# Performance work log

Measured on AMD Instinct MI355X. Metric: run time of the kernel, lower is better.

Reference implementation:

```python
import jax, jax.numpy as jnp
import numpy as np

B, S, H, V, T = 32, 128, 256, 32000, 100


def setup_inputs() -> dict:
    key = jax.random.key(0)
    ks = jax.random.split(key, 16)
    s = 1.0 / np.sqrt(H)

    def u(k, shape):
        return jax.random.uniform(k, shape, jnp.float32, -s, s)

    return dict(
        enc_outputs=jax.random.normal(ks[0], (B, S, H), jnp.float32),
        enc_hidden=jax.random.normal(ks[1], (1, B, H), jnp.float32),
        target_tensor=jax.random.randint(ks[2], (B, T), 0, V),
        embedding=u(ks[3], (V, H)),
        Qw=u(ks[4], (H, H)), Qb=u(ks[5], (H,)),
        Kw=u(ks[6], (H, H)), Kb=u(ks[7], (H,)),
        Vw=u(ks[8], (1, H)), Vb=u(ks[9], (1,)),
        W_ih=u(ks[10], (3 * H, 2 * H)), W_hh=u(ks[11], (3 * H, H)),
        b_ih=u(ks[12], (3 * H,)), b_hh=u(ks[13], (3 * H,)),
        out_w=u(ks[14], (V, H)), out_b=u(ks[15], (V,)),
    )


def reference(enc_outputs, enc_hidden, target_tensor, embedding,
              Qw, Qb, Kw, Kb, Vw, Vb, W_ih, W_hh, b_ih, b_hh, out_w, out_b):
    # Teacher-forcing decode: dec_input starts at token 0, then target[:, i].
    Bv, Sv, Hd = enc_outputs.shape
    Tv = target_tensor.shape[1]
    # K(keys) is step-invariant: precompute once (same math as in-loop Linear).
    enc_k = enc_outputs @ Kw.T + Kb  # (B,S,H)
    tokens = jnp.concatenate(
        [jnp.zeros((Bv, 1), target_tensor.dtype), target_tensor[:, :-1]], axis=1)
    tokens_t = tokens.T  # (T,B)

    def step(h, tok):
        emb = embedding[tok]                                  # (B,H), dropout=eval noop
        q = h @ Qw.T + Qb                                     # query from hidden
        e = jnp.tanh(q[:, None, :] + enc_k)                   # (B,S,H) additive attn
        scores = jnp.einsum('bsh,h->bs', e, Vw[0]) + Vb[0]    # (B,S)
        w = jax.nn.softmax(scores, axis=-1)
        ctx = jnp.einsum('bs,bsh->bh', w, enc_outputs)        # bmm(weights, keys)
        x = jnp.concatenate([emb, ctx], axis=-1)              # (B,2H)
        gi = x @ W_ih.T + b_ih
        gh = h @ W_hh.T + b_hh
        r = jax.nn.sigmoid(gi[:, :Hd] + gh[:, :Hd])
        z = jax.nn.sigmoid(gi[:, Hd:2 * Hd] + gh[:, Hd:2 * Hd])
        n = jnp.tanh(gi[:, 2 * Hd:] + r * gh[:, 2 * Hd:])
        h_new = (1.0 - z) * n + z * h                         # torch GRU cell
        logits = h_new @ out_w.T + out_b                      # (B,V)
        return h_new, (logits, w)

    h_final, (logits, atts) = jax.lax.scan(step, enc_hidden[0], tokens_t)
    dec_outputs = jax.nn.log_softmax(jnp.transpose(logits, (1, 0, 2)), axis=-1)  # (B,T,V)
    atts = jnp.transpose(atts, (1, 0, 2))                     # (B,T,S)
    return dec_outputs, h_final[None], atts
```

## Files before the change

kernel.cpp:

```cpp
#include <hip/hip_runtime.h>
#include <hip/hip_bf16.h>

#define Bn 32
#define Sn 128
#define Hn 256
#define Vn 32000
#define Tn 100
#define GIn 768
#define AGENT __HIP_MEMORY_SCOPE_AGENT

typedef __attribute__((ext_vector_type(8))) short bf16x8;
typedef __attribute__((ext_vector_type(4))) float f32x4;

__device__ __forceinline__ float frcp(float x){ return __builtin_amdgcn_rcpf(x); }
__device__ __forceinline__ float ftanh(float x){ return 1.0f - 2.0f*frcp(__expf(2.0f*x)+1.0f); }
__device__ __forceinline__ float fsigm(float x){ return frcp(1.0f + __expf(-x)); }
__device__ __forceinline__ float b2f(unsigned short u){
  unsigned int v = ((unsigned int)u) << 16; return __builtin_bit_cast(float, v);
}
__device__ __forceinline__ unsigned short f2bu(float f){
  unsigned int u = __builtin_bit_cast(unsigned int, f);
  u += 0x7FFFu + ((u >> 16) & 1u);
  return (unsigned short)(u >> 16);
}
__device__ __forceinline__ void st_ag_u(unsigned int* p, unsigned int v){
  __hip_atomic_store(p, v, __ATOMIC_RELAXED, AGENT);
}
__device__ __forceinline__ unsigned int ld_ag_u(unsigned int* p){
  return __hip_atomic_load(p, __ATOMIC_RELAXED, AGENT);
}

__global__ __launch_bounds__(256) void k_tr(const float* __restrict__ in,
    float* __restrict__ out, int R, int C)
{
  __shared__ float tile[32][33];
  const int bx = blockIdx.x*32, by = blockIdx.y*32;
  const int tx = threadIdx.x & 31, ty = threadIdx.x >> 5;
  #pragma unroll
  for(int r = ty; r < 32; r += 8)
    if(by + r < R && bx + tx < C) tile[r][tx] = in[(size_t)(by + r)*C + bx + tx];
  __syncthreads();
  #pragma unroll
  for(int r = ty; r < 32; r += 8)
    if(bx + r < C && by + tx < R) out[(size_t)(bx + r)*R + by + tx] = tile[tx][r];
}

__global__ __launch_bounds__(256) void k_packW1R(const float* __restrict__ Qw,
    const float* __restrict__ Whh, unsigned short* __restrict__ W1R)
{
  const int tid = blockIdx.x*256 + threadIdx.x;
  const int lane = tid & 63;
  const int fragid = tid >> 6;
  const int tt = fragid % 5;
  const int kk = (fragid/5) % 8;
  const int w  = (fragid/40) % 8;
  const int hb = fragid/320;
  const int lr = lane & 15, lg = lane >> 4;
  const float* src;
  if(tt < 2){
    const int f = w*32 + tt*16 + lr;
    src = Qw + (size_t)f*Hn;
  } else {
    const int lf = w*48 + (tt-2)*16 + lr;
    const int g = lf >> 7, jj = lf & 127;
    src = Whh + (size_t)(g*256 + hb*128 + jj)*Hn;
  }
  const int col = kk*32 + lg*8;
  float4 v0 = *(const float4*)(src + col), v1 = *(const float4*)(src + col + 4);
  unsigned short* d = W1R + ((size_t)fragid*64 + lane)*8;
  d[0]=f2bu(v0.x); d[1]=f2bu(v0.y); d[2]=f2bu(v0.z); d[3]=f2bu(v0.w);
  d[4]=f2bu(v1.x); d[5]=f2bu(v1.y); d[6]=f2bu(v1.z); d[7]=f2bu(v1.w);
}

__global__ __launch_bounds__(256) void k_cvt(const float* __restrict__ src,
    __hip_bfloat16* __restrict__ dst, int n)
{
  int i = (blockIdx.x*256 + threadIdx.x)*4;
  if(i < n){
    float4 v = *(const float4*)(src + i);
    dst[i+0] = __float2bfloat16(v.x);
    dst[i+1] = __float2bfloat16(v.y);
    dst[i+2] = __float2bfloat16(v.z);
    dst[i+3] = __float2bfloat16(v.w);
  }
}

__global__ __launch_bounds__(256) void k_enc2(const float* __restrict__ enc_outputs,
    const float* __restrict__ KwT, const float* __restrict__ Kb,
    unsigned short* __restrict__ enc_kb16)
{
  const int r0 = blockIdx.x*16, j = threadIdx.x;
  __shared__ __align__(16) float encl[Hn][20];
  #pragma unroll
  for(int r = 0; r < 16; r++) encl[j][r] = enc_outputs[(size_t)(r0 + r)*Hn + j];
  __syncthreads();
  float acc[16];
  #pragma unroll
  for(int r = 0; r < 16; r++) acc[r] = Kb[j];
  for(int d = 0; d < Hn; d++){
    const float wv = KwT[(size_t)d*Hn + j];
    const float4 e0 = *(const float4*)&encl[d][0];
    const float4 e1 = *(const float4*)&encl[d][4];
    const float4 e2 = *(const float4*)&encl[d][8];
    const float4 e3 = *(const float4*)&encl[d][12];
    acc[0]+=e0.x*wv; acc[1]+=e0.y*wv; acc[2]+=e0.z*wv; acc[3]+=e0.w*wv;
    acc[4]+=e1.x*wv; acc[5]+=e1.y*wv; acc[6]+=e1.z*wv; acc[7]+=e1.w*wv;
    acc[8]+=e2.x*wv; acc[9]+=e2.y*wv; acc[10]+=e2.z*wv; acc[11]+=e2.w*wv;
    acc[12]+=e3.x*wv; acc[13]+=e3.y*wv; acc[14]+=e3.z*wv; acc[15]+=e3.w*wv;
  }
  #pragma unroll
  for(int r = 0; r < 16; r++) enc_kb16[(size_t)(r0 + r)*Hn + j] = f2bu(acc[r]);
}

__global__ __launch_bounds__(256) void k_packEk(const unsigned short* __restrict__ enc_kb16,
    unsigned short* __restrict__ ekP)
{
  const int tid = blockIdx.x*256 + threadIdx.x;
  const int b = tid >> 12;
  const int o = tid & 4095;
  const int g = o >> 6, l = o & 63;
  const int w = g >> 3, i = g & 7;
  const int s = w*16 + (l >> 2);
  const int e0 = i*32 + (l & 3)*8;
  const int4 v = *(const int4*)(enc_kb16 + ((size_t)(b*Sn + s))*Hn + e0);
  *(int4*)(ekP + (size_t)b*32768 + (size_t)o*8) = v;
}

__global__ __launch_bounds__(768) void k_encW2b(const float* __restrict__ enc_outputs,
    const float* __restrict__ W_ihT, unsigned short* __restrict__ encW2P)
{
  const int r0 = blockIdx.x*16, tid = threadIdx.x;
  __shared__ __align__(16) float encl[Hn][20];
  if(tid < Hn){
    #pragma unroll
    for(int r = 0; r < 16; r++) encl[tid][r] = enc_outputs[(size_t)(r0 + r)*Hn + tid];
  }
  __syncthreads();
  float acc[16];
  #pragma unroll
  for(int r = 0; r < 16; r++) acc[r] = 0.f;
  for(int d = 0; d < Hn; d++){
    const float wv = W_ihT[(size_t)(Hn + d)*GIn + tid];
    const float4 e0 = *(const float4*)&encl[d][0];
    const float4 e1 = *(const float4*)&encl[d][4];
    const float4 e2 = *(const float4*)&encl[d][8];
    const float4 e3 = *(const float4*)&encl[d][12];
    acc[0]+=e0.x*wv; acc[1]+=e0.y*wv; acc[2]+=e0.z*wv; acc[3]+=e0.w*wv;
    acc[4]+=e1.x*wv; acc[5]+=e1.y*wv; acc[6]+=e1.z*wv; acc[7]+=e1.w*wv;
    acc[8]+=e2.x*wv; acc[9]+=e2.y*wv; acc[10]+=e2.z*wv; acc[11]+=e2.w*wv;
    acc[12]+=e3.x*wv; acc[13]+=e3.y*wv; acc[14]+=e3.z*wv; acc[15]+=e3.w*wv;
  }
  const int g = tid >> 8, jj = tid & 255;
  const int hb = jj >> 7, c = g*128 + (jj & 127);
  #pragma unroll
  for(int r = 0; r < 16; r++){
    const int bs = r0 + r;
    const int bb = bs >> 7, ss = bs & 127;
    encW2P[(((size_t)bb*2 + hb)*384 + c)*128 + ss] = f2bu(acc[r]);
  }
}

__global__ __launch_bounds__(768) void k_giemb2(const int* __restrict__ target,
    const float* __restrict__ embedding, const float* __restrict__ W_ihT,
    const float* __restrict__ b_ih, float* __restrict__ gi_emb)
{
  const int r0 = blockIdx.x*16, tid = threadIdx.x;
  __shared__ __align__(16) float embl[Hn][20];
  if(tid < Hn){
    #pragma unroll
    for(int r = 0; r < 16; r++){
      const int row = r0 + r;
      const int t = row >> 5, b = row & 31;
      const int tok = (t == 0) ? 0 : target[b*Tn + (t-1)];
      embl[tid][r] = embedding[(size_t)tok*Hn + tid];
    }
  }
  __syncthreads();
  float acc[16];
  #pragma unroll
  for(int r = 0; r < 16; r++) acc[r] = b_ih[tid];
  for(int d = 0; d < Hn; d++){
    const float wv = W_ihT[(size_t)d*GIn + tid];
    const float4 e0 = *(const float4*)&embl[d][0];
    const float4 e1 = *(const float4*)&embl[d][4];
    const float4 e2 = *(const float4*)&embl[d][8];
    const float4 e3 = *(const float4*)&embl[d][12];
    acc[0]+=e0.x*wv; acc[1]+=e0.y*wv; acc[2]+=e0.z*wv; acc[3]+=e0.w*wv;
    acc[4]+=e1.x*wv; acc[5]+=e1.y*wv; acc[6]+=e1.z*wv; acc[7]+=e1.w*wv;
    acc[8]+=e2.x*wv; acc[9]+=e2.y*wv; acc[10]+=e2.z*wv; acc[11]+=e2.w*wv;
    acc[12]+=e3.x*wv; acc[13]+=e3.y*wv; acc[14]+=e3.z*wv; acc[15]+=e3.w*wv;
  }
  #pragma unroll
  for(int r = 0; r < 16; r++) gi_emb[(size_t)(r0 + r)*GIn + tid] = acc[r];
}

__global__ __launch_bounds__(512, 2) void k_loop5(
    const float* __restrict__ enc_hidden,
    const unsigned short* __restrict__ ekP,
    const unsigned short* __restrict__ encW2P,
    const unsigned short* __restrict__ W1R,
    const float* __restrict__ Qb, const float* __restrict__ b_hh,
    const float* __restrict__ Vw, const float* __restrict__ Vb,
    const float* __restrict__ gi_emb,
    __hip_bfloat16* __restrict__ h_all,
    float* __restrict__ atts_out,
    float* __restrict__ hfin_out,
    unsigned int* hbuf,
    unsigned int* hflag)
{
  const int p = blockIdx.x >> 1, hb = blockIdx.x & 1, b = p;
  const int tid = threadIdx.x;
  const int lane = tid & 63, wv = tid >> 6;
  const int lr = lane & 15, lg = lane >> 4;

  __shared__ __align__(16) unsigned short ek_l[32768];
  __shared__ __align__(16) unsigned short ew_l[32768];
  __shared__ __align__(16) float h_sh[128];
  __shared__ __align__(16) short h_b16[Hn];
  __shared__ __align__(16) float qgh_sh[1024];
  __shared__ __align__(16) float vw_sh[Hn];
  __shared__ __align__(16) float sc_sh[Sn];
  __shared__ __align__(16) float w_sh[Sn];
  __shared__ __align__(16) float gic_l[384];

  {
    const unsigned short* src = ekP + (size_t)b*32768;
    #pragma unroll
    for(int c = 0; c < 8; c++){
      const int idx = (c*512 + tid)*8;
      *(int4*)(ek_l + idx) = *(const int4*)(src + idx);
    }
  }
  {
    const unsigned short* src = encW2P + ((size_t)(b*2 + hb)*384)*128;
    #pragma unroll
    for(int i = 0; i < 8; i++){
      const int id = i*512 + tid;
      const int c = id >> 4, sg = id & 15;
      *(int4*)(ew_l + c*128 + ((sg ^ (c & 15)) << 3)) =
          *(const int4*)(src + (size_t)c*128 + sg*8);
    }
  }
  bf16x8 er0, er1, er2, er3;
  {
    const unsigned short* esrc = encW2P +
        ((size_t)((b*2 + hb)*384 + 256 + (tid >> 2)))*128 + (tid & 3)*32;
    er0 = *(const bf16x8*)(esrc);
    er1 = *(const bf16x8*)(esrc + 8);
    er2 = *(const bf16x8*)(esrc + 16);
    er3 = *(const bf16x8*)(esrc + 24);
  }
  bf16x8 w1f[40];
  {
    const unsigned short* wsrc = W1R + (((size_t)(hb*8 + wv)*40)*64 + lane)*8;
    #pragma unroll
    for(int f = 0; f < 40; f++) w1f[f] = *(const bf16x8*)(wsrc + (size_t)f*512);
  }
  float bias_r[5]; int idx_r[5];
  #pragma unroll
  for(int tt = 0; tt < 2; tt++){
    const int f = wv*32 + tt*16 + lr;
    bias_r[tt] = Qb[f]; idx_r[tt] = f;
  }
  #pragma unroll
  for(int tt = 2; tt < 5; tt++){
    const int lf = wv*48 + (tt-2)*16 + lr;
    const int g = lf >> 7, jj = lf & 127;
    bias_r[tt] = b_hh[g*256 + hb*128 + jj];
    idx_r[tt]  = 256 + g*256 + hb*128 + jj;
  }
  if(tid < Hn){
    float hv = enc_hidden[b*Hn + tid];
    h_b16[tid] = (short)f2bu(hv);
    vw_sh[tid] = Vw[tid];
  }
  if(tid < 128) h_sh[tid] = enc_hidden[b*Hn + hb*128 + tid];
  __syncthreads();
  const float vb0 = Vb[0];
  const int s2 = tid >> 2, g2 = tid & 3;

  for(int t = 0; t < Tn; t++){
    const int par = t & 1;
    {
      f32x4 acc[5];
      #pragma unroll
      for(int tt = 0; tt < 5; tt++) acc[tt] = (f32x4){0.f,0.f,0.f,0.f};
      #pragma unroll
      for(int kk = 0; kk < 8; kk++){
        bf16x8 a = *(const bf16x8*)(h_b16 + kk*32 + lg*8);
        #pragma unroll
        for(int tt = 0; tt < 5; tt++)
          acc[tt] = __builtin_amdgcn_mfma_f32_16x16x32_bf16(a, w1f[kk*5 + tt], acc[tt], 0, 0, 0);
      }
      if(lane < 16){
        #pragma unroll
        for(int tt = 0; tt < 5; tt++)
          qgh_sh[idx_r[tt]] = acc[tt][0] + bias_r[tt];
      }
    }
    __syncthreads();

    {
      float pacc = 0.f;
      #pragma unroll
      for(int i = 0; i < 8; i++){
        bf16x8 e8 = *(const bf16x8*)(ek_l + ((wv*8 + i) << 9) + lane*8);
        const int kb = i*32 + g2*8;
        #pragma unroll
        for(int j = 0; j < 8; j++){
          float ev = b2f((unsigned short)e8[j]);
          pacc = fmaf(vw_sh[kb + j], ftanh(qgh_sh[kb + j] + ev), pacc);
        }
      }
      pacc += __shfl_xor(pacc, 1); pacc += __shfl_xor(pacc, 2);
      if(g2 == 0) sc_sh[s2] = pacc + vb0;
    }
    __syncthreads();

    if(tid < 64){
      float v0 = sc_sh[tid], v1 = sc_sh[tid + 64];
      float m = fmaxf(v0, v1);
      #pragma unroll
      for(int off = 1; off < 64; off <<= 1) m = fmaxf(m, __shfl_xor(m, off));
      float e0 = __expf(v0 - m), e1 = __expf(v1 - m);
      float sm = e0 + e1;
      #pragma unroll
      for(int off = 1; off < 64; off <<= 1) sm += __shfl_xor(sm, off);
      float inv = frcp(sm);
      float w0 = e0*inv, w1 = e1*inv;
      w_sh[tid] = w0; w_sh[tid + 64] = w1;
      if(hb == 0){
        float* ao = atts_out + ((size_t)b*Tn + t)*Sn;
        ao[tid] = w0; ao[tid + 64] = w1;
      }
    }
    __syncthreads();

    float ge0 = 0.f, ge1 = 0.f, ge2 = 0.f;
    if(tid < 128){
      const float* ge = gi_emb + ((size_t)t*Bn + b)*GIn + hb*128 + tid;
      ge0 = ge[0]; ge1 = ge[256]; ge2 = ge[512];
    }

    {
      const int c3 = tid >> 1, s3 = tid & 1;
      float a3 = 0.f;
      #pragma unroll
      for(int i = 0; i < 8; i++){
        bf16x8 e = *(const bf16x8*)(ew_l + c3*128 + ((((s3 << 3) + i) ^ (c3 & 15)) << 3));
        const float4 wa = *(const float4*)&w_sh[s3*64 + i*8];
        const float4 wb = *(const float4*)&w_sh[s3*64 + i*8 + 4];
        a3 = fmaf(wa.x, b2f((unsigned short)e[0]), a3);
        a3 = fmaf(wa.y, b2f((unsigned short)e[1]), a3);
        a3 = fmaf(wa.z, b2f((unsigned short)e[2]), a3);
        a3 = fmaf(wa.w, b2f((unsigned short)e[3]), a3);
        a3 = fmaf(wb.x, b2f((unsigned short)e[4]), a3);
        a3 = fmaf(wb.y, b2f((unsigned short)e[5]), a3);
        a3 = fmaf(wb.z, b2f((unsigned short)e[6]), a3);
        a3 = fmaf(wb.w, b2f((unsigned short)e[7]), a3);
      }
      a3 += __shfl_xor(a3, 1);
      if(!(tid & 1)) gic_l[c3] = a3;
      const float* wq = &w_sh[(tid & 3)*32];
      float r2 = 0.f;
      #pragma unroll
      for(int j = 0; j < 8; j++) r2 = fmaf(wq[j],      b2f((unsigned short)er0[j]), r2);
      #pragma unroll
      for(int j = 0; j < 8; j++) r2 = fmaf(wq[8 + j],  b2f((unsigned short)er1[j]), r2);
      #pragma unroll
      for(int j = 0; j < 8; j++) r2 = fmaf(wq[16 + j], b2f((unsigned short)er2[j]), r2);
      #pragma unroll
      for(int j = 0; j < 8; j++) r2 = fmaf(wq[24 + j], b2f((unsigned short)er3[j]), r2);
      r2 += __shfl_xor(r2, 1); r2 += __shfl_xor(r2, 2);
      if(!(tid & 3)) gic_l[256 + (tid >> 2)] = r2;
    }
    __syncthreads();

    if(tid < 128){
      float gr = ge0 + gic_l[tid];
      float gz = ge1 + gic_l[128 + tid];
      float gn = ge2 + gic_l[256 + tid];
      const int jg = hb*128 + tid;
      float r = fsigm(gr + qgh_sh[256 + jg]);
      float z = fsigm(gz + qgh_sh[512 + jg]);
      float n = ftanh(gn + r*qgh_sh[768 + jg]);
      float hn2 = (1.0f - z)*n + z*h_sh[tid];
      h_sh[tid] = hn2;
      const unsigned short hb16 = f2bu(hn2);
      h_b16[jg] = (short)hb16;
      h_all[((size_t)t*Bn + b)*Hn + jg] = __float2bfloat16(hn2);
      if(t == Tn-1) hfin_out[b*Hn + jg] = hn2;
      if(t < Tn-1){
        float hnx = __shfl_down(hn2, 1);
        if(!(tid & 1)){
          unsigned int u = (unsigned int)hb16 | ((unsigned int)f2bu(hnx) << 16);
          st_ag_u(&hbuf[((size_t)(par*32 + p)*2 + hb)*64 + (tid >> 1)], u);
        }
      }
    }
    __syncthreads();

    if(t < Tn-1){
      if(tid == 0){
        __hip_atomic_store(&hflag[p*2 + hb], (unsigned)(t + 1), __ATOMIC_RELEASE, AGENT);
        long cnt = 0;
        while(__hip_atomic_load(&hflag[p*2 + (hb^1)], __ATOMIC_ACQUIRE, AGENT) < (unsigned)(t + 1)
              && ++cnt < 10000000L){}
      }
      __syncthreads();
      if(tid < 64){
        unsigned int u = ld_ag_u(&hbuf[((size_t)(par*32 + p)*2 + (hb^1))*64 + tid]);
        ((unsigned int*)h_b16)[(hb^1)*64 + tid] = u;
      }
      __syncthreads();
    }
  }
}

__global__ __launch_bounds__(512, 2) void k_logits2(
    const short* __restrict__ h_all, const short* __restrict__ w_bf,
    const float* __restrict__ out_b,
    float* __restrict__ pmax, float* __restrict__ psum,
    const float* __restrict__ lse, float* __restrict__ dec_out,
    int pass)
{
  const int tid = threadIdx.x;
  const int wave = tid >> 6, lane = tid & 63;
  const int lr = lane & 15, lg = lane >> 4;
  const int wm = wave >> 2, wn = wave & 3;
  const int n0 = blockIdx.x*256 + wn*64;
  const int m0 = blockIdx.y*256 + wm*128;
  f32x4 acc[8][4];
  #pragma unroll
  for(int mt = 0; mt < 8; mt++)
    #pragma unroll
    for(int nt = 0; nt < 4; nt++) acc[mt][nt] = (f32x4){0.f,0.f,0.f,0.f};
  #pragma unroll
  for(int kk = 0; kk < 8; kk++){
    bf16x8 am[8], bn[4];
    #pragma unroll
    for(int mt = 0; mt < 8; mt++){
      int row = m0 + mt*16 + lr; row = row < 3200 ? row : 3199;
      am[mt] = *(const bf16x8*)(h_all + (size_t)row*Hn + kk*32 + lg*8);
    }
    #pragma unroll
    for(int nt = 0; nt < 4; nt++)
      bn[nt] = *(const bf16x8*)(w_bf + (size_t)(n0 + nt*16 + lr)*Hn + kk*32 + lg*8);
    #pragma unroll
    for(int mt = 0; mt < 8; mt++)
      #pragma unroll
      for(int nt = 0; nt < 4; nt++)
        acc[mt][nt] = __builtin_amdgcn_mfma_f32_16x16x32_bf16(am[mt], bn[nt], acc[mt][nt], 0, 0, 0);
  }
  float bias[4];
  #pragma unroll
  for(int nt = 0; nt < 4; nt++) bias[nt] = out_b[n0 + nt*16 + lr];

  if(pass == 0){
    __shared__ float pm_l[256][4];
    __shared__ float ps_l[256][4];
    #pragma unroll
    for(int mt = 0; mt < 8; mt++){
      #pragma unroll
      for(int i = 0; i < 4; i++){
        float v0 = acc[mt][0][i] + bias[0], v1 = acc[mt][1][i] + bias[1];
        float v2 = acc[mt][2][i] + bias[2], v3 = acc[mt][3][i] + bias[3];
        float m = fmaxf(fmaxf(v0, v1), fmaxf(v2, v3));
        m = fmaxf(m, __shfl_xor(m, 1)); m = fmaxf(m, __shfl_xor(m, 2));
        m = fmaxf(m, __shfl_xor(m, 4)); m = fmaxf(m, __shfl_xor(m, 8));
        float s = __expf(v0 - m) + __expf(v1 - m) + __expf(v2 - m) + __expf(v3 - m);
        s += __shfl_xor(s, 1); s += __shfl_xor(s, 2);
        s += __shfl_xor(s, 4); s += __shfl_xor(s, 8);
        if(lr == 0){
          const int rl = wm*128 + mt*16 + lg*4 + i;
          pm_l[rl][wn] = m; ps_l[rl][wn] = s;
        }
      }
    }
    __syncthreads();
    if(tid < 256){
      const int rg = blockIdx.y*256 + tid;
      if(rg < 3200){
        float m = fmaxf(fmaxf(pm_l[tid][0], pm_l[tid][1]), fmaxf(pm_l[tid][2], pm_l[tid][3]));
        float s = ps_l[tid][0]*__expf(pm_l[tid][0] - m) + ps_l[tid][1]*__expf(pm_l[tid][1] - m)
                + ps_l[tid][2]*__expf(pm_l[tid][2] - m) + ps_l[tid][3]*__expf(pm_l[tid][3] - m);
        pmax[(size_t)blockIdx.x*3200 + rg] = m;
        psum[(size_t)blockIdx.x*3200 + rg] = s;
      }
    }
  } else {
    #pragma unroll
    for(int mt = 0; mt < 8; mt++){
      #pragma unroll
      for(int i = 0; i < 4; i++){
        const int rg = blockIdx.y*256 + wm*128 + mt*16 + lg*4 + i;
        if(rg < 3200){
          const float l = lse[rg];
          const int bb = rg & 31, tt2 = rg >> 5;
          float* dst = dec_out + (size_t)bb*((size_t)Tn*Vn) + (size_t)tt2*Vn + n0;
          dst[ 0 + lr] = acc[mt][0][i] + bias[0] - l;
          dst[16 + lr] = acc[mt][1][i] + bias[1] - l;
          dst[32 + lr] = acc[mt][2][i] + bias[2] - l;
          dst[48 + lr] = acc[mt][3][i] + bias[3] - l;
        }
      }
    }
  }
}

__global__ __launch_bounds__(256) void k_lse(const float* __restrict__ pmax,
    const float* __restrict__ psum, float* __restrict__ lse)
{
  const int row = blockIdx.x*256 + threadIdx.x;
  if(row >= Tn*Bn) return;
  float m = -3.0e38f;
  for(int c = 0; c < 125; c++) m = fmaxf(m, pmax[(size_t)c*3200 + row]);
  float s = 0.f;
  for(int c = 0; c < 125; c++)
    s += psum[(size_t)c*3200 + row] * __expf(pmax[(size_t)c*3200 + row] - m);
  lse[row] = m + __logf(s);
}

extern "C" void kernel_launch(void* const* d_in, const int* in_sizes, int n_in,
                              void* d_out, int out_size, void* d_ws, size_t ws_size,
                              hipStream_t stream)
{
  const float* enc_outputs = (const float*)d_in[0];
  const float* enc_hidden  = (const float*)d_in[1];
  const int*   target      = (const int*)d_in[2];
  const float* embedding   = (const float*)d_in[3];
  const float* Qw   = (const float*)d_in[4];
  const float* Qb   = (const float*)d_in[5];
  const float* Kw   = (const float*)d_in[6];
  const float* Kb   = (const float*)d_in[7];
  const float* Vw   = (const float*)d_in[8];
  const float* Vb   = (const float*)d_in[9];
  const float* W_ih = (const float*)d_in[10];
  const float* W_hh = (const float*)d_in[11];
  const float* b_ih = (const float*)d_in[12];
  const float* b_hh = (const float*)d_in[13];
  const float* out_w = (const float*)d_in[14];
  const float* out_b = (const float*)d_in[15];

  float* dec  = (float*)d_out;
  float* hfin = dec + (size_t)Bn*Tn*Vn;
  float* atts = hfin + Bn*Hn;

  unsigned short* enc_kb16 = (unsigned short*)(dec);
  unsigned short* ekP      = (unsigned short*)(dec + 524288);
  unsigned short* encW2P   = (unsigned short*)(dec + 1048576);
  float* gi_emb = dec + 2621440;
  float* W_ihT  = dec + 5079040;
  float* KwT    = dec + 5472256;
  float* pmax   = dec + 5537792;
  float* psum   = dec + 5937792;
  unsigned short* W1R = (unsigned short*)(dec + 6337792);
  unsigned int* hbuf  = (unsigned int*)(dec + 6501632);
  unsigned int* hflag = (unsigned int*)(dec + 6509824);

  float* wsf = (float*)d_ws;
  float* lse = wsf;
  __hip_bfloat16* h_all = (__hip_bfloat16*)(wsf + 3200);
  __hip_bfloat16* w_bf  = h_all + (size_t)Tn*Bn*Hn;

  k_tr     <<<dim3(8, 8),   dim3(256), 0, stream>>>(Kw, KwT, 256, 256);
  k_tr     <<<dim3(16, 24), dim3(256), 0, stream>>>(W_ih, W_ihT, 768, 512);
  k_packW1R<<<dim3(160),    dim3(256), 0, stream>>>(Qw, W_hh, W1R);
  k_cvt    <<<dim3((Vn*Hn)/1024), dim3(256), 0, stream>>>(out_w, w_bf, Vn*Hn);
  k_enc2   <<<dim3(256), dim3(256), 0, stream>>>(enc_outputs, KwT, Kb, enc_kb16);
  k_packEk <<<dim3(512), dim3(256), 0, stream>>>(enc_kb16, ekP);
  k_encW2b <<<dim3(256), dim3(768), 0, stream>>>(enc_outputs, W_ihT, encW2P);
  k_giemb2 <<<dim3(200), dim3(768), 0, stream>>>(target, embedding, W_ihT, b_ih, gi_emb);

  hipMemsetAsync((void*)hflag, 0, 64*sizeof(unsigned int), stream);

  k_loop5 <<<dim3(64), dim3(512), 0, stream>>>(enc_hidden, ekP, encW2P, W1R,
            Qb, b_hh, Vw, Vb, gi_emb, h_all, atts, hfin, hbuf, hflag);

  k_logits2<<<dim3(125, 13), dim3(512), 0, stream>>>(
            (const short*)h_all, (const short*)w_bf, out_b,
            pmax, psum, (const float*)nullptr, (float*)nullptr, 0);
  k_lse    <<<dim3(13), dim3(256), 0, stream>>>(pmax, psum, lse);
  k_logits2<<<dim3(125, 13), dim3(512), 0, stream>>>(
            (const short*)h_all, (const short*)w_bf, out_b,
            (float*)nullptr, (float*)nullptr, lse, dec, 1);
}
```

Before: 1.373 ms.

## Split attention scores across block pair and use MFMA for context projection

Each pair of blocks now splits the 128 sequence positions so each block computes attention scores for 64 positions, exchanging partial scores through a global buffer with a second flag. The hidden-state exchange is moved so the local half of the Q/W_hh matvec runs before waiting on the partner, overlapping the sync with compute. The context-times-W_ih projection is recast as MFMA over a fragment-packed layout, which removes the packEk kernel. Block-to-pair mapping is also permuted so paired blocks sit further apart. The change adds a second cross-block handshake per step in exchange for halving the tanh work.

After: 2.068 ms. +50.6%, slower.

```diff
diff --git a/kernel.cpp b/kernel.cpp
--- a/kernel.cpp
+++ b/kernel.cpp
@@ -112,22 +112,8 @@
   for(int r = 0; r < 16; r++) enc_kb16[(size_t)(r0 + r)*Hn + j] = f2bu(acc[r]);
 }
 
-__global__ __launch_bounds__(256) void k_packEk(const unsigned short* __restrict__ enc_kb16,
-    unsigned short* __restrict__ ekP)
-{
-  const int tid = blockIdx.x*256 + threadIdx.x;
-  const int b = tid >> 12;
-  const int o = tid & 4095;
-  const int g = o >> 6, l = o & 63;
-  const int w = g >> 3, i = g & 7;
-  const int s = w*16 + (l >> 2);
-  const int e0 = i*32 + (l & 3)*8;
-  const int4 v = *(const int4*)(enc_kb16 + ((size_t)(b*Sn + s))*Hn + e0);
-  *(int4*)(ekP + (size_t)b*32768 + (size_t)o*8) = v;
-}
-
-__global__ __launch_bounds__(768) void k_encW2b(const float* __restrict__ enc_outputs,
-    const float* __restrict__ W_ihT, unsigned short* __restrict__ encW2P)
+__global__ __launch_bounds__(768) void k_encW2F(const float* __restrict__ enc_outputs,
+    const float* __restrict__ W_ihT, unsigned short* __restrict__ encW2F)
 {
   const int r0 = blockIdx.x*16, tid = threadIdx.x;
   __shared__ __align__(16) float encl[Hn][20];
@@ -151,12 +137,17 @@
     acc[12]+=e3.x*wv; acc[13]+=e3.y*wv; acc[14]+=e3.z*wv; acc[15]+=e3.w*wv;
   }
   const int g = tid >> 8, jj = tid & 255;
-  const int hb = jj >> 7, c = g*128 + (jj & 127);
+  const int hb = jj >> 7, jl = jj & 127;
+  const int c = g*128 + jl;
+  const int wvv = c/48, rem = c - wvv*48, tt = rem >> 4, lr = rem & 15;
   #pragma unroll
   for(int r = 0; r < 16; r++){
     const int bs = r0 + r;
-    const int bb = bs >> 7, ss = bs & 127;
-    encW2P[(((size_t)bb*2 + hb)*384 + c)*128 + ss] = f2bu(acc[r]);
+    const int bb = bs >> 7, s = bs & 127;
+    const int kk = s >> 5, lg = (s >> 3) & 3, e = s & 7;
+    const int lane = lg*16 + lr;
+    encW2F[(size_t)(bb*2 + hb)*49152 + (size_t)((wvv*12 + tt*4 + kk)*64 + lane)*8 + e]
+        = f2bu(acc[r]);
   }
 }
 
@@ -194,10 +185,10 @@
   for(int r = 0; r < 16; r++) gi_emb[(size_t)(r0 + r)*GIn + tid] = acc[r];
 }
 
-__global__ __launch_bounds__(512, 2) void k_loop5(
+__global__ __launch_bounds__(512, 2) void k_loop6(
     const float* __restrict__ enc_hidden,
-    const unsigned short* __restrict__ ekP,
-    const unsigned short* __restrict__ encW2P,
+    const unsigned short* __restrict__ enc_kb16,
+    const unsigned short* __restrict__ encW2F,
     const unsigned short* __restrict__ W1R,
     const float* __restrict__ Qb, const float* __restrict__ b_hh,
     const float* __restrict__ Vw, const float* __restrict__ Vb,
@@ -206,49 +197,44 @@
     float* __restrict__ atts_out,
     float* __restrict__ hfin_out,
     unsigned int* hbuf,
-    unsigned int* hflag)
-{
-  const int p = blockIdx.x >> 1, hb = blockIdx.x & 1, b = p;
+    unsigned int* sbuf,
+    unsigned int* hflag,
+    unsigned int* sflag)
+{
+  const int bid = blockIdx.x;
+  const int hb = (bid >> 3) & 1;
+  const int p  = (bid & 7) | ((bid >> 4) << 3);
+  const int b = p;
   const int tid = threadIdx.x;
   const int lane = tid & 63, wv = tid >> 6;
   const int lr = lane & 15, lg = lane >> 4;
 
-  __shared__ __align__(16) unsigned short ek_l[32768];
-  __shared__ __align__(16) unsigned short ew_l[32768];
+  __shared__ __align__(16) unsigned short ek_l[64*256];
+  __shared__ __align__(16) unsigned short ew_l[49152];
   __shared__ __align__(16) float h_sh[128];
-  __shared__ __align__(16) short h_b16[Hn];
+  __shared__ __align__(16) unsigned short hown_l[128];
   __shared__ __align__(16) float qgh_sh[1024];
   __shared__ __align__(16) float vw_sh[Hn];
   __shared__ __align__(16) float sc_sh[Sn];
   __shared__ __align__(16) float w_sh[Sn];
+  __shared__ __align__(16) unsigned short wb_l[Sn];
   __shared__ __align__(16) float gic_l[384];
 
   {
-    const unsigned short* src = ekP + (size_t)b*32768;
-    #pragma unroll
-    for(int c = 0; c < 8; c++){
+    const unsigned short* src = enc_kb16 + ((size_t)b*Sn + hb*64)*Hn;
+    #pragma unroll
+    for(int c = 0; c < 4; c++){
       const int idx = (c*512 + tid)*8;
       *(int4*)(ek_l + idx) = *(const int4*)(src + idx);
     }
   }
   {
-    const unsigned short* src = encW2P + ((size_t)(b*2 + hb)*384)*128;
-    #pragma unroll
-    for(int i = 0; i < 8; i++){
-      const int id = i*512 + tid;
-      const int c = id >> 4, sg = id & 15;
-      *(int4*)(ew_l + c*128 + ((sg ^ (c & 15)) << 3)) =
-          *(const int4*)(src + (size_t)c*128 + sg*8);
-    }
-  }
-  bf16x8 er0, er1, er2, er3;
-  {
-    const unsigned short* esrc = encW2P +
-        ((size_t)((b*2 + hb)*384 + 256 + (tid >> 2)))*128 + (tid & 3)*32;
-    er0 = *(const bf16x8*)(esrc);
-    er1 = *(const bf16x8*)(esrc + 8);
-    er2 = *(const bf16x8*)(esrc + 16);
-    er3 = *(const bf16x8*)(esrc + 24);
+    const unsigned short* src = encW2F + (size_t)(b*2 + hb)*49152;
+    #pragma unroll
+    for(int c = 0; c < 12; c++){
+      const int idx = (c*512 + tid)*8;
+      *(int4*)(ew_l + idx) = *(const int4*)(src + idx);
+    }
   }
   bf16x8 w1f[40];
   {
@@ -269,56 +255,107 @@
     bias_r[tt] = b_hh[g*256 + hb*128 + jj];
     idx_r[tt]  = 256 + g*256 + hb*128 + jj;
   }
-  if(tid < Hn){
-    float hv = enc_hidden[b*Hn + tid];
-    h_b16[tid] = (short)f2bu(hv);
-    vw_sh[tid] = Vw[tid];
-  }
-  if(tid < 128) h_sh[tid] = enc_hidden[b*Hn + hb*128 + tid];
+  if(tid < Hn) vw_sh[tid] = Vw[tid];
+  if(tid < 128){
+    float hv = enc_hidden[b*Hn + hb*128 + tid];
+    h_sh[tid] = hv; hown_l[tid] = f2bu(hv);
+  }
+  if(tid < 64){
+    float h0 = enc_hidden[b*Hn + hb*128 + tid*2];
+    float h1 = enc_hidden[b*Hn + hb*128 + tid*2 + 1];
+    unsigned int u = (unsigned int)f2bu(h0) | ((unsigned int)f2bu(h1) << 16);
+    st_ag_u(&hbuf[((size_t)(0*32 + p)*2 + hb)*64 + tid], u);
+  }
   __syncthreads();
+  if(tid == 0)
+    __hip_atomic_store(&hflag[p*2 + hb], 1u, __ATOMIC_RELEASE, AGENT);
+
   const float vb0 = Vb[0];
-  const int s2 = tid >> 2, g2 = tid & 3;
+  const int sl = wv*8 + (lane >> 3), g2 = lane & 7;
+  const unsigned short* ekrow = ek_l + sl*256 + g2*32;
 
   for(int t = 0; t < Tn; t++){
     const int par = t & 1;
+    f32x4 acc[5];
+    #pragma unroll
+    for(int tt = 0; tt < 5; tt++) acc[tt] = (f32x4){0.f,0.f,0.f,0.f};
+    #pragma unroll
+    for(int kkl = 0; kkl < 4; kkl++){
+      bf16x8 a = *(const bf16x8*)(hown_l + kkl*32 + lg*8);
+      const int kf = (hb*4 + kkl)*5;
+      #pragma unroll
+      for(int tt = 0; tt < 5; tt++)
+        acc[tt] = __builtin_amdgcn_mfma_f32_16x16x32_bf16(a, w1f[kf + tt], acc[tt], 0, 0, 0);
+    }
     {
-      f32x4 acc[5];
-      #pragma unroll
-      for(int tt = 0; tt < 5; tt++) acc[tt] = (f32x4){0.f,0.f,0.f,0.f};
-      #pragma unroll
-      for(int kk = 0; kk < 8; kk++){
-        bf16x8 a = *(const bf16x8*)(h_b16 + kk*32 + lg*8);
+      long cnt = 0;
+      while(__hip_atomic_load(&hflag[p*2 + (hb^1)], __ATOMIC_ACQUIRE, AGENT) < (unsigned)(t + 1)
+            && ++cnt < 10000000L){}
+    }
+    {
+      unsigned int* hsrc = hbuf + ((size_t)(par*32 + p)*2 + (hb^1))*64;
+      #pragma unroll
+      for(int kkl = 0; kkl < 4; kkl++){
+        unsigned int u0 = ld_ag_u(hsrc + kkl*16 + lg*4);
+        unsigned int u1 = ld_ag_u(hsrc + kkl*16 + lg*4 + 1);
+        unsigned int u2 = ld_ag_u(hsrc + kkl*16 + lg*4 + 2);
+        unsigned int u3 = ld_ag_u(hsrc + kkl*16 + lg*4 + 3);
+        bf16x8 a;
+        a[0]=(short)(u0&0xFFFF); a[1]=(short)(u0>>16);
+        a[2]=(short)(u1&0xFFFF); a[3]=(short)(u1>>16);
+        a[4]=(short)(u2&0xFFFF); a[5]=(short)(u2>>16);
+        a[6]=(short)(u3&0xFFFF); a[7]=(short)(u3>>16);
+        const int kf = ((1-hb)*4 + kkl)*5;
         #pragma unroll
         for(int tt = 0; tt < 5; tt++)
-          acc[tt] = __builtin_amdgcn_mfma_f32_16x16x32_bf16(a, w1f[kk*5 + tt], acc[tt], 0, 0, 0);
-      }
-      if(lane < 16){
-        #pragma unroll
-        for(int tt = 0; tt < 5; tt++)
-          qgh_sh[idx_r[tt]] = acc[tt][0] + bias_r[tt];
-      }
+          acc[tt] = __builtin_amdgcn_mfma_f32_16x16x32_bf16(a, w1f[kf + tt], acc[tt], 0, 0, 0);
+      }
+    }
+    if(lane < 16){
+      #pragma unroll
+      for(int tt = 0; tt < 5; tt++)
+        qgh_sh[idx_r[tt]] = acc[tt][0] + bias_r[tt];
     }
     __syncthreads();
 
     {
       float pacc = 0.f;
       #pragma unroll
-      for(int i = 0; i < 8; i++){
-        bf16x8 e8 = *(const bf16x8*)(ek_l + ((wv*8 + i) << 9) + lane*8);
-        const int kb = i*32 + g2*8;
+      for(int c = 0; c < 4; c++){
+        bf16x8 e8 = *(const bf16x8*)(ekrow + c*8);
+        const int kb = g2*32 + c*8;
         #pragma unroll
         for(int j = 0; j < 8; j++){
           float ev = b2f((unsigned short)e8[j]);
           pacc = fmaf(vw_sh[kb + j], ftanh(qgh_sh[kb + j] + ev), pacc);
         }
       }
-      pacc += __shfl_xor(pacc, 1); pacc += __shfl_xor(pacc, 2);
-      if(g2 == 0) sc_sh[s2] = pacc + vb0;
+      pacc += __shfl_xor(pacc, 1); pacc += __shfl_xor(pacc, 2); pacc += __shfl_xor(pacc, 4);
+      if(g2 == 0){
+        const float sv = pacc + vb0;
+        sc_sh[hb*64 + sl] = sv;
+        st_ag_u(&sbuf[((size_t)(par*32 + p)*2 + hb)*64 + sl],
+                __builtin_bit_cast(unsigned int, sv));
+      }
+    }
+    float ge0 = 0.f, ge1 = 0.f, ge2 = 0.f;
+    if(tid < 128){
+      const float* ge = gi_emb + ((size_t)t*Bn + b)*GIn + hb*128 + tid;
+      ge0 = ge[0]; ge1 = ge[256]; ge2 = ge[512];
     }
     __syncthreads();
+    if(tid == 0)
+      __hip_atomic_store(&sflag[p*2 + hb], (unsigned)(t + 1), __ATOMIC_RELEASE, AGENT);
 
     if(tid < 64){
-      float v0 = sc_sh[tid], v1 = sc_sh[tid + 64];
+      long cnt = 0;
+      while(__hip_atomic_load(&sflag[p*2 + (hb^1)], __ATOMIC_ACQUIRE, AGENT) < (unsigned)(t + 1)
+            && ++cnt < 10000000L){}
+      unsigned int uo = ld_ag_u(&sbuf[((size_t)(par*32 + p)*2 + (hb^1))*64 + tid]);
+      float vo = __builtin_bit_cast(float, uo);
+      float vmine = sc_sh[hb*64 + tid];
+      float v0 = hb ? vo : vmine;
+      float v1 = hb ? vmine : vo;
       float m = fmaxf(v0, v1);
       #pragma unroll
       for(int off = 1; off < 64; off <<= 1) m = fmaxf(m, __shfl_xor(m, off));
@@ -329,6 +366,7 @@
       float inv = frcp(sm);
       float w0 = e0*inv, w1 = e1*inv;
       w_sh[tid] = w0; w_sh[tid + 64] = w1;
+      wb_l[tid] = f2bu(w0); wb_l[tid + 64] = f2bu(w1);
       if(hb == 0){
         float* ao = atts_out + ((size_t)b*Tn + t)*Sn;
         ao[tid] = w0; ao[tid + 64] = w1;
@@ -336,43 +374,21 @@
     }
     __syncthreads();
 
-    float ge0 = 0.f, ge1 = 0.f, ge2 = 0.f;
-    if(tid < 128){
-      const float* ge = gi_emb + ((size_t)t*Bn + b)*GIn + hb*128 + tid;
-      ge0 = ge[0]; ge1 = ge[256]; ge2 = ge[512];
-    }
-
     {
-      const int c3 = tid >> 1, s3 = tid & 1;
-      float a3 = 0.f;
-      #pragma unroll
-      for(int i = 0; i < 8; i++){
-        bf16x8 e = *(const bf16x8*)(ew_l + c3*128 + ((((s3 << 3) + i) ^ (c3 & 15)) << 3));
-        const float4 wa = *(const float4*)&w_sh[s3*64 + i*8];
-        const float4 wb = *(const float4*)&w_sh[s3*64 + i*8 + 4];
-        a3 = fmaf(wa.x, b2f((unsigned short)e[0]), a3);
-        a3 = fmaf(wa.y, b2f((unsigned short)e[1]), a3);
-        a3 = fmaf(wa.z, b2f((unsigned short)e[2]), a3);
-        a3 = fmaf(wa.w, b2f((unsigned short)e[3]), a3);
-        a3 = fmaf(wb.x, b2f((unsigned short)e[4]), a3);
-        a3 = fmaf(wb.y, b2f((unsigned short)e[5]), a3);
-        a3 = fmaf(wb.z, b2f((unsigned short)e[6]), a3);
-        a3 = fmaf(wb.w, b2f((unsigned short)e[7]), a3);
-      }
-      a3 += __shfl_xor(a3, 1);
-      if(!(tid & 1)) gic_l[c3] = a3;
-      const float* wq = &w_sh[(tid & 3)*32];
-      float r2 = 0.f;
-      #pragma unroll
-      for(int j = 0; j < 8; j++) r2 = fmaf(wq[j],      b2f((unsigned short)er0[j]), r2);
-      #pragma unroll
-      for(int j = 0; j < 8; j++) r2 = fmaf(wq[8 + j],  b2f((unsigned short)er1[j]), r2);
-      #pragma unroll
-      for(int j = 0; j < 8; j++) r2 = fmaf(wq[16 + j], b2f((unsigned short)er2[j]), r2);
-      #pragma unroll
-      for(int j = 0; j < 8; j++) r2 = fmaf(wq[24 + j], b2f((unsigned short)er3[j]), r2);
-      r2 += __shfl_xor(r2, 1); r2 += __shfl_xor(r2, 2);
-      if(!(tid & 3)) gic_l[256 + (tid >> 2)] = r2;
+      bf16x8 wfrag[4];
+      #pragma unroll
+      for(int kk = 0; kk < 4; kk++)
+        wfrag[kk] = *(const bf16x8*)(wb_l + kk*32 + lg*8);
+      #pragma unroll
+      for(int tt = 0; tt < 3; tt++){
+        f32x4 a3 = (f32x4){0.f,0.f,0.f,0.f};
+        #pragma unroll
+        for(int kk = 0; kk < 4; kk++){
+          bf16x8 bfr = *(const bf16x8*)(ew_l + (size_t)((wv*12 + tt*4 + kk)*64 + lane)*8);
+          a3 = __builtin_amdgcn_mfma_f32_16x16x32_bf16(wfrag[kk], bfr, a3, 0, 0, 0);
+        }
+        if(lane < 16) gic_l[wv*48 + tt*16 + lane] = a3[0];
+      }
     }
     __syncthreads();
 
@@ -387,33 +403,20 @@
       float hn2 = (1.0f - z)*n + z*h_sh[tid];
       h_sh[tid] = hn2;
       const unsigned short hb16 = f2bu(hn2);
-      h_b16[jg] = (short)hb16;
+      hown_l[tid] = hb16;
       h_all[((size_t)t*Bn + b)*Hn + jg] = __float2bfloat16(hn2);
       if(t == Tn-1) hfin_out[b*Hn + jg] = hn2;
       if(t < Tn-1){
         float hnx = __shfl_down(hn2, 1);
         if(!(tid & 1)){
           unsigned int u = (unsigned int)hb16 | ((unsigned int)f2bu(hnx) << 16);
-          st_ag_u(&hbuf[((size_t)(par*32 + p)*2 + hb)*64 + (tid >> 1)], u);
+          st_ag_u(&hbuf[((size_t)(((t+1)&1)*32 + p)*2 + hb)*64 + (tid >> 1)], u);
         }
       }
     }
     __syncthreads();
-
-    if(t < Tn-1){
-      if(tid == 0){
-        __hip_atomic_store(&hflag[p*2 + hb], (unsigned)(t + 1), __ATOMIC_RELEASE, AGENT);
-        long cnt = 0;
-        while(__hip_atomic_load(&hflag[p*2 + (hb^1)], __ATOMIC_ACQUIRE, AGENT) < (unsigned)(t + 1)
-              && ++cnt < 10000000L){}
-      }
-      __syncthreads();
-      if(tid < 64){
-        unsigned int u = ld_ag_u(&hbuf[((size_t)(par*32 + p)*2 + (hb^1))*64 + tid]);
-        ((unsigned int*)h_b16)[(hb^1)*64 + tid] = u;
-      }
-      __syncthreads();
-    }
+    if(tid == 0 && t < Tn-1)
+      __hip_atomic_store(&hflag[p*2 + hb], (unsigned)(t + 2), __ATOMIC_RELEASE, AGENT);
   }
 }
 
@@ -547,16 +550,17 @@
   float* atts = hfin + Bn*Hn;
 
   unsigned short* enc_kb16 = (unsigned short*)(dec);
-  unsigned short* ekP      = (unsigned short*)(dec + 524288);
-  unsigned short* encW2P   = (unsigned short*)(dec + 1048576);
-  float* gi_emb = dec + 2621440;
-  float* W_ihT  = dec + 5079040;
-  float* KwT    = dec + 5472256;
-  float* pmax   = dec + 5537792;
-  float* psum   = dec + 5937792;
-  unsigned short* W1R = (unsigned short*)(dec + 6337792);
-  unsigned int* hbuf  = (unsigned int*)(dec + 6501632);
-  unsigned int* hflag = (unsigned int*)(dec + 6509824);
+  unsigned short* encW2F   = (unsigned short*)(dec + 524288);
+  float* gi_emb = dec + 2097152;
+  float* W_ihT  = dec + 4554752;
+  float* KwT    = dec + 4947968;
+  float* pmax   = dec + 5013504;
+  float* psum   = dec + 5413504;
+  unsigned short* W1R = (unsigned short*)(dec + 5813504);
+  unsigned int* hbuf  = (unsigned int*)(dec + 5977344);
+  unsigned int* sbuf  = (unsigned int*)(dec + 5985536);
+  unsigned int* hflag = (unsigned int*)(dec + 5993728);
+  unsigned int* sflag = hflag + 64;
 
   float* wsf = (float*)d_ws;
   float* lse = wsf;
@@ -568,14 +572,13 @@
   k_packW1R<<<dim3(160),    dim3(256), 0, stream>>>(Qw, W_hh, W1R);
   k_cvt    <<<dim3((Vn*Hn)/1024), dim3(256), 0, stream>>>(out_w, w_bf, Vn*Hn);
   k_enc2   <<<dim3(256), dim3(256), 0, stream>>>(enc_outputs, KwT, Kb, enc_kb16);
-  k_packEk <<<dim3(512), dim3(256), 0, stream>>>(enc_kb16, ekP);
-  k_encW2b <<<dim3(256), dim3(768), 0, stream>>>(enc_outputs, W_ihT, encW2P);
+  k_encW2F <<<dim3(256), dim3(768), 0, stream>>>(enc_outputs, W_ihT, encW2F);
   k_giemb2 <<<dim3(200), dim3(768), 0, stream>>>(target, embedding, W_ihT, b_ih, gi_emb);
 
-  hipMemsetAsync((void*)hflag, 0, 64*sizeof(unsigned int), stream);
-
-  k_loop5 <<<dim3(64), dim3(512), 0, stream>>>(enc_hidden, ekP, encW2P, W1R,
-            Qb, b_hh, Vw, Vb, gi_emb, h_all, atts, hfin, hbuf, hflag);
+  hipMemsetAsync((void*)hflag, 0, 128*sizeof(unsigned int), stream);
+
+  k_loop6 <<<dim3(64), dim3(512), 0, stream>>>(enc_hidden, enc_kb16, encW2F, W1R,
+            Qb, b_hh, Vw, Vb, gi_emb, h_all, atts, hfin, hbuf, sbuf, hflag, sflag);
 
   k_logits2<<<dim3(125, 13), dim3(512), 0, stream>>>(
             (const short*)h_all, (const short*)w_bf, out_b,
```

## Use MFMA for context-gate matvec, keep enc keys in registers, remap blocks

Applied to the files above, without the earlier changes.

Precomputes the encoder-times-W_ih context projection in an MFMA fragment layout so the per-step gate contribution is computed with bf16 16x16x32 MFMAs from bf16 attention weights, replacing the scalar FMA path and the register-held slice. Encoder keys move from LDS into per-thread registers, and LDS holds only the enlarged fragment buffer. Blocks are remapped so the two half-blocks of each batch land 8 apart, and the flag wait is folded into the first wave, removing a barrier. Attention weights are now rounded to bf16 before the context product, which costs some precision and adds register pressure.

New measurement: 1.400 ms. No clear change (+2.0%).

```diff
diff --git a/kernel.cpp b/kernel.cpp
--- a/kernel.cpp
+++ b/kernel.cpp
@@ -126,8 +126,8 @@
   *(int4*)(ekP + (size_t)b*32768 + (size_t)o*8) = v;
 }
 
-__global__ __launch_bounds__(768) void k_encW2b(const float* __restrict__ enc_outputs,
-    const float* __restrict__ W_ihT, unsigned short* __restrict__ encW2P)
+__global__ __launch_bounds__(768) void k_encW2F(const float* __restrict__ enc_outputs,
+    const float* __restrict__ W_ihT, unsigned short* __restrict__ encW2F)
 {
   const int r0 = blockIdx.x*16, tid = threadIdx.x;
   __shared__ __align__(16) float encl[Hn][20];
@@ -151,12 +151,17 @@
     acc[12]+=e3.x*wv; acc[13]+=e3.y*wv; acc[14]+=e3.z*wv; acc[15]+=e3.w*wv;
   }
   const int g = tid >> 8, jj = tid & 255;
-  const int hb = jj >> 7, c = g*128 + (jj & 127);
+  const int hb = jj >> 7, jl = jj & 127;
+  const int c = g*128 + jl;
+  const int wvv = c/48, rem = c - wvv*48, tt = rem >> 4, lr = rem & 15;
   #pragma unroll
   for(int r = 0; r < 16; r++){
     const int bs = r0 + r;
-    const int bb = bs >> 7, ss = bs & 127;
-    encW2P[(((size_t)bb*2 + hb)*384 + c)*128 + ss] = f2bu(acc[r]);
+    const int bb = bs >> 7, s = bs & 127;
+    const int kk = s >> 5, lg = (s >> 3) & 3, e = s & 7;
+    const int lane = lg*16 + lr;
+    encW2F[(size_t)(bb*2 + hb)*49152 + (size_t)((wvv*12 + tt*4 + kk)*64 + lane)*8 + e]
+        = f2bu(acc[r]);
   }
 }
 
@@ -194,10 +199,10 @@
   for(int r = 0; r < 16; r++) gi_emb[(size_t)(r0 + r)*GIn + tid] = acc[r];
 }
 
-__global__ __launch_bounds__(512, 2) void k_loop5(
+__global__ __launch_bounds__(512, 2) void k_loop7(
     const float* __restrict__ enc_hidden,
     const unsigned short* __restrict__ ekP,
-    const unsigned short* __restrict__ encW2P,
+    const unsigned short* __restrict__ encW2F,
     const unsigned short* __restrict__ W1R,
     const float* __restrict__ Qb, const float* __restrict__ b_hh,
     const float* __restrict__ Vw, const float* __restrict__ Vb,
@@ -208,47 +213,37 @@
     unsigned int* hbuf,
     unsigned int* hflag)
 {
-  const int p = blockIdx.x >> 1, hb = blockIdx.x & 1, b = p;
+  const int bid = blockIdx.x;
+  const int hb = (bid >> 3) & 1;
+  const int p  = (bid & 7) | ((bid >> 4) << 3);
+  const int b = p;
   const int tid = threadIdx.x;
   const int lane = tid & 63, wv = tid >> 6;
   const int lr = lane & 15, lg = lane >> 4;
 
-  __shared__ __align__(16) unsigned short ek_l[32768];
-  __shared__ __align__(16) unsigned short ew_l[32768];
+  __shared__ __align__(16) unsigned short ew_l[49152];
   __shared__ __align__(16) float h_sh[128];
   __shared__ __align__(16) short h_b16[Hn];
   __shared__ __align__(16) float qgh_sh[1024];
   __shared__ __align__(16) float vw_sh[Hn];
   __shared__ __align__(16) float sc_sh[Sn];
-  __shared__ __align__(16) float w_sh[Sn];
+  __shared__ __align__(16) unsigned short wb_l[Sn];
   __shared__ __align__(16) float gic_l[384];
 
   {
-    const unsigned short* src = ekP + (size_t)b*32768;
-    #pragma unroll
-    for(int c = 0; c < 8; c++){
+    const unsigned short* src = encW2F + (size_t)(b*2 + hb)*49152;
+    #pragma unroll
+    for(int c = 0; c < 12; c++){
       const int idx = (c*512 + tid)*8;
-      *(int4*)(ek_l + idx) = *(const int4*)(src + idx);
-    }
-  }
+      *(int4*)(ew_l + idx) = *(const int4*)(src + idx);
+    }
+  }
+  bf16x8 ekr[8];
   {
-    const unsigned short* src = encW2P + ((size_t)(b*2 + hb)*384)*128;
-    #pragma unroll
-    for(int i = 0; i < 8; i++){
-      const int id = i*512 + tid;
-      const int c = id >> 4, sg = id & 15;
-      *(int4*)(ew_l + c*128 + ((sg ^ (c & 15)) << 3)) =
-          *(const int4*)(src + (size_t)c*128 + sg*8);
-    }
-  }
-  bf16x8 er0, er1, er2, er3;
-  {
-    const unsigned short* esrc = encW2P +
-        ((size_t)((b*2 + hb)*384 + 256 + (tid >> 2)))*128 + (tid & 3)*32;
-    er0 = *(const bf16x8*)(esrc);
-    er1 = *(const bf16x8*)(esrc + 8);
-    er2 = *(const bf16x8*)(esrc + 16);
-    er3 = *(const bf16x8*)(esrc + 24);
+    const unsigned short* esrc = ekP + (size_t)b*32768;
+    #pragma unroll
+    for(int i = 0; i < 8; i++)
+      ekr[i] = *(const bf16x8*)(esrc + (size_t)((wv*8 + i)*64 + lane)*8);
   }
   bf16x8 w1f[40];
   {
@@ -270,14 +265,13 @@
     idx_r[tt]  = 256 + g*256 + hb*128 + jj;
   }
   if(tid < Hn){
-    float hv = enc_hidden[b*Hn + tid];
-    h_b16[tid] = (short)f2bu(hv);
     vw_sh[tid] = Vw[tid];
+    h_b16[tid] = (short)f2bu(enc_hidden[b*Hn + tid]);
   }
   if(tid < 128) h_sh[tid] = enc_hidden[b*Hn + hb*128 + tid];
   __syncthreads();
   const float vb0 = Vb[0];
-  const int s2 = tid >> 2, g2 = tid & 3;
+  const int g2 = tid & 3;
 
   for(int t = 0; t < Tn; t++){
     const int par = t & 1;
@@ -304,7 +298,7 @@
       float pacc = 0.f;
       #pragma unroll
       for(int i = 0; i < 8; i++){
-        bf16x8 e8 = *(const bf16x8*)(ek_l + ((wv*8 + i) << 9) + lane*8);
+        const bf16x8 e8 = ekr[i];
         const int kb = i*32 + g2*8;
         #pragma unroll
         for(int j = 0; j < 8; j++){
@@ -313,7 +307,7 @@
         }
       }
       pacc += __shfl_xor(pacc, 1); pacc += __shfl_xor(pacc, 2);
-      if(g2 == 0) sc_sh[s2] = pacc + vb0;
+      if(g2 == 0) sc_sh[tid >> 2] = pacc + vb0;
     }
     __syncthreads();
 
@@ -328,51 +322,34 @@
       for(int off = 1; off < 64; off <<= 1) sm += __shfl_xor(sm, off);
       float inv = frcp(sm);
       float w0 = e0*inv, w1 = e1*inv;
-      w_sh[tid] = w0; w_sh[tid + 64] = w1;
+      wb_l[tid] = f2bu(w0); wb_l[tid + 64] = f2bu(w1);
       if(hb == 0){
         float* ao = atts_out + ((size_t)b*Tn + t)*Sn;
         ao[tid] = w0; ao[tid + 64] = w1;
       }
     }
-    __syncthreads();
-
     float ge0 = 0.f, ge1 = 0.f, ge2 = 0.f;
     if(tid < 128){
       const float* ge = gi_emb + ((size_t)t*Bn + b)*GIn + hb*128 + tid;
       ge0 = ge[0]; ge1 = ge[256]; ge2 = ge[512];
     }
+    __syncthreads();
 
     {
-      const int c3 = tid >> 1, s3 = tid & 1;
-      float a3 = 0.f;
-      #pragma unroll
-      for(int i = 0; i < 8; i++){
-        bf16x8 e = *(const bf16x8*)(ew_l + c3*128 + ((((s3 << 3) + i) ^ (c3 & 15)) << 3));
-        const float4 wa = *(const float4*)&w_sh[s3*64 + i*8];
-        const float4 wb = *(const float4*)&w_sh[s3*64 + i*8 + 4];
-        a3 = fmaf(wa.x, b2f((unsigned short)e[0]), a3);
-        a3 = fmaf(wa.y, b2f((unsigned short)e[1]), a3);
-        a3 = fmaf(wa.z, b2f((unsigned short)e[2]), a3);
-        a3 = fmaf(wa.w, b2f((unsigned short)e[3]), a3);
-        a3 = fmaf(wb.x, b2f((unsigned short)e[4]), a3);
-        a3 = fmaf(wb.y, b2f((unsigned short)e[5]), a3);
-        a3 = fmaf(wb.z, b2f((unsigned short)e[6]), a3);
-        a3 = fmaf(wb.w, b2f((unsigned short)e[7]), a3);
-      }
-      a3 += __shfl_xor(a3, 1);
-      if(!(tid & 1)) gic_l[c3] = a3;
-      const float* wq = &w_sh[(tid & 3)*32];
-      float r2 = 0.f;
-      #pragma unroll
-      for(int j = 0; j < 8; j++) r2 = fmaf(wq[j],      b2f((unsigned short)er0[j]), r2);
-      #pragma unroll
-      for(int j = 0; j < 8; j++) r2 = fmaf(wq[8 + j],  b2f((unsigned short)er1[j]), r2);
-      #pragma unroll
-      for(int j = 0; j < 8; j++) r2 = fmaf(wq[16 + j], b2f((unsigned short)er2[j]), r2);
-      #pragma unroll
-      for(int j = 0; j < 8; j++) r2 = fmaf(wq[24 + j], b2f((unsigned short)er3[j]), r2);
-      r2 += __shfl_xor(r2, 1); r2 += __shfl_xor(r2, 2);
-      if(!(tid & 3)) gic_l[256 + (tid >> 2)] = r2;
+      bf16x8 wfrag[4];
+      #pragma unroll
+      for(int kk = 0; kk < 4; kk++)
+        wfrag[kk] = *(const bf16x8*)(wb_l + kk*32 + lg*8);
+      #pragma unroll
+      for(int tt = 0; tt < 3; tt++){
+        f32x4 a3 = (f32x4){0.f,0.f,0.f,0.f};
+        #pragma unroll
+        for(int kk = 0; kk < 4; kk++){
+          bf16x8 bfr = *(const bf16x8*)(ew_l + (size_t)((wv*12 + tt*4 + kk)*64 + lane)*8);
+          a3 = __builtin_amdgcn_mfma_f32_16x16x32_bf16(wfrag[kk], bfr, a3, 0, 0, 0);
+        }
+        if(lane < 16) gic_l[wv*48 + tt*16 + lane] = a3[0];
+      }
     }
     __syncthreads();
 
@@ -401,14 +378,12 @@
     __syncthreads();
 
     if(t < Tn-1){
-      if(tid == 0){
+      if(tid == 0)
         __hip_atomic_store(&hflag[p*2 + hb], (unsigned)(t + 1), __ATOMIC_RELEASE, AGENT);
+      if(tid < 64){
         long cnt = 0;
         while(__hip_atomic_load(&hflag[p*2 + (hb^1)], __ATOMIC_ACQUIRE, AGENT) < (unsigned)(t + 1)
               && ++cnt < 10000000L){}
-      }
-      __syncthreads();
-      if(tid < 64){
         unsigned int u = ld_ag_u(&hbuf[((size_t)(par*32 + p)*2 + (hb^1))*64 + tid]);
         ((unsigned int*)h_b16)[(hb^1)*64 + tid] = u;
       }
@@ -548,7 +523,7 @@
 
   unsigned short* enc_kb16 = (unsigned short*)(dec);
   unsigned short* ekP      = (unsigned short*)(dec + 524288);
-  unsigned short* encW2P   = (unsigned short*)(dec + 1048576);
+  unsigned short* encW2F   = (unsigned short*)(dec + 1048576);
   float* gi_emb = dec + 2621440;
   float* W_ihT  = dec + 5079040;
   float* KwT    = dec + 5472256;
@@ -569,12 +544,12 @@
   k_cvt    <<<dim3((Vn*Hn)/1024), dim3(256), 0, stream>>>(out_w, w_bf, Vn*Hn);
   k_enc2   <<<dim3(256), dim3(256), 0, stream>>>(enc_outputs, KwT, Kb, enc_kb16);
   k_packEk <<<dim3(512), dim3(256), 0, stream>>>(enc_kb16, ekP);
-  k_encW2b <<<dim3(256), dim3(768), 0, stream>>>(enc_outputs, W_ihT, encW2P);
+  k_encW2F <<<dim3(256), dim3(768), 0, stream>>>(enc_outputs, W_ihT, encW2F);
   k_giemb2 <<<dim3(200), dim3(768), 0, stream>>>(target, embedding, W_ihT, b_ih, gi_emb);
 
   hipMemsetAsync((void*)hflag, 0, 64*sizeof(unsigned int), stream);
 
-  k_loop5 <<<dim3(64), dim3(512), 0, stream>>>(enc_hidden, ekP, encW2P, W1R,
+  k_loop7 <<<dim3(64), dim3(512), 0, stream>>>(enc_hidden, ekP, encW2F, W1R,
             Qb, b_hh, Vw, Vb, gi_emb, h_all, atts, hfin, hbuf, hflag);
 
   k_logits2<<<dim3(125, 13), dim3(512), 0, stream>>>(
```
